# Kernel optimization log

Hardware: AMD Instinct MI355X
Metric: run time of the kernel (lower is better)

Reference implementation:

```python
import jax, jax.numpy as jnp
import numpy as np

S, B, K, H = 2048, 256, 64, 128  # seq_len, batch, process_dim, hidden_size


def softplus10(x):
    return jax.nn.softplus(10.0 * x) / 10.0


def setup_inputs() -> dict:
    key = jax.random.key(0)
    ks = jax.random.split(key, 10)
    sc = 0.1
    dt = jax.random.uniform(ks[0], (S, B), dtype=jnp.float32)
    seq_types = jax.random.randint(ks[1], (S, B), 0, K)  # in [0, K); K is padding idx
    h0 = jnp.zeros((B, H), dtype=jnp.float32)
    embed_W = jax.random.normal(ks[2], (K + 1, K), dtype=jnp.float32) * sc
    embed_W = embed_W.at[K].set(0.0)  # padding_idx row is zero
    W_ih = jax.random.normal(ks[3], (H, K), dtype=jnp.float32) * sc
    b_ih = jax.random.normal(ks[4], (H,), dtype=jnp.float32) * sc
    W_hh = jax.random.normal(ks[5], (H, H), dtype=jnp.float32) * sc
    b_hh = jax.random.normal(ks[6], (H,), dtype=jnp.float32) * sc
    dec_W = jax.random.normal(ks[7], (H, K + H), dtype=jnp.float32) * sc
    dec_b = jax.random.normal(ks[8], (H,), dtype=jnp.float32) * sc
    return {"dt": dt, "h0": h0, "embed_W": embed_W, "W_ih": W_ih, "b_ih": b_ih,
            "W_hh": W_hh, "b_hh": b_hh, "dec_W": dec_W, "dec_b": dec_b,
            "seq_types": seq_types}


def reference(dt, h0, embed_W, W_ih, b_ih, W_hh, b_hh, dec_W, dec_b, seq_types):
    # Per-event recurrence: h(t) = hidden_i * exp(-decay_i * dt_i)
    def step(h, inp):
        dt_t, ty_t = inp                     # [B], [B]
        x = embed_W[ty_t]                    # [B, K] embedding lookup
        concat = jnp.concatenate([x, h], axis=1)          # [B, K+H]
        decay = softplus10(concat @ dec_W.T + dec_b)      # [B, H]
        hidden = jnp.tanh(x @ W_ih.T + b_ih + h @ W_hh.T + b_hh)  # RNNCell tanh
        h_new = hidden * jnp.exp(-decay * dt_t[:, None])  # decayed hidden state
        return h_new, (hidden, decay, h_new)

    _, (hiddens, decays, hiddens_ti) = jax.lax.scan(step, h0, (dt, seq_types))
    # each: [S, B, H], matching the per-step lists of the torch module
    return hiddens, decays, hiddens_ti
```

## Files before the change

kernel.cpp:

```cpp
#include <hip/hip_runtime.h>

#define SEQ 2048
#define BAT 256
#define KD  64
#define HD  128
#define SBH 67108864u

typedef _Float16 half2v  __attribute__((ext_vector_type(2)));
typedef __fp16   fp16x2  __attribute__((ext_vector_type(2)));

template<int PAT>
__device__ __forceinline__ float swz(float x) {
    return __int_as_float(__builtin_amdgcn_ds_swizzle(__float_as_int(x), PAT));
}
#define XOR4 0x101F

template<int CTRL>
__device__ __forceinline__ float dpp_add(float keep, float send) {
    const int r = __builtin_amdgcn_update_dpp(0, __float_as_int(send),
                                              CTRL, 0xF, 0xF, true);
    return keep + __int_as_float(r);
}
template<int CTRL>
__device__ __forceinline__ float dpp_mov(float send) {
    const int r = __builtin_amdgcn_update_dpp(0, __float_as_int(send),
                                              CTRL, 0xF, 0xF, true);
    return __int_as_float(r);
}

__device__ __forceinline__ int PK(float a, float b) {
    fp16x2 p = __builtin_amdgcn_cvt_pkrtz(a, b);
    return __builtin_bit_cast(int, p);
}

__device__ __forceinline__ float fdot2(int w, int h, float c) {
#if __has_builtin(__builtin_amdgcn_fdot2)
    return __builtin_amdgcn_fdot2(__builtin_bit_cast(half2v, w),
                                  __builtin_bit_cast(half2v, h), c, false);
#else
    half2v wv = __builtin_bit_cast(half2v, w), hv = __builtin_bit_cast(half2v, h);
    return fmaf((float)wv[1], (float)hv[1], fmaf((float)wv[0], (float)hv[0], c));
#endif
}

#define PIN(x) asm volatile("" : "+v"(x))
#define PIN4(v4) PIN(v4.x); PIN(v4.y); PIN(v4.z); PIN(v4.w)

#define STEP_BARRIER() do {                                   \
    asm volatile("s_waitcnt lgkmcnt(0)" ::: "memory");        \
    __builtin_amdgcn_s_barrier();                             \
    asm volatile("" ::: "memory");                            \
} while (0)

__global__ __launch_bounds__(128) void precompute_tables(
    const float* __restrict__ embed_W, const float* __restrict__ W_ih,
    const float* __restrict__ b_ih,    const float* __restrict__ b_hh,
    const float* __restrict__ dec_W,   const float* __restrict__ dec_b,
    float* __restrict__ tabH, float* __restrict__ tabD)
{
    __shared__ float x[KD];
    const int ty = blockIdx.x;
    const int r  = threadIdx.x;
    if (r < KD) x[r] = embed_W[ty * KD + r];
    __syncthreads();
    float ah = 0.f, ad = 0.f;
#pragma unroll
    for (int k = 0; k < KD; ++k) {
        const float xv = x[k];
        ah += xv * W_ih[r * KD + k];
        ad += xv * dec_W[r * (KD + HD) + k];
    }
    tabH[ty * HD + r] = ah + b_ih[r] + b_hh[r];
    tabD[ty * HD + r] = ad + dec_b[r];
}

__global__ __launch_bounds__(256, 1) void hawkes_rnn(
    const float* __restrict__ dt_g,  const float* __restrict__ h0,
    const float* __restrict__ W_hh,  const float* __restrict__ dec_W,
    const int*   __restrict__ seq_types,
    const float* __restrict__ tabH,  const float* __restrict__ tabD,
    float* __restrict__ out)
{
    __shared__ __align__(16) _Float16 h16[2][HD];
    __shared__ __align__(8) int2 dtty[SEQ + 2];

    const int b    = blockIdx.x;
    const int tid  = threadIdx.x;
    const int lane = tid & 63;
    const int b0 = lane & 1, b1 = (lane >> 1) & 1;
    const int b2 = (lane >> 2) & 1, b3 = (lane >> 3) & 1;
    const int g    = (tid >> 6) * 4 + (lane >> 4);
    const int row  = 8 * g + 4 * b0 + 2 * b1 + b2;
    const int chunk = b0 | (b1 << 1) | (b2 << 2);

    for (int t = tid; t < SEQ; t += 256) {
        dtty[t] = make_int2(__float_as_int(dt_g[(size_t)t * BAT + b]),
                            seq_types[(size_t)t * BAT + b]);
    }
    if (tid < 2) dtty[SEQ + tid] = make_int2(0, 0);
    if (tid < HD) h16[0][tid] = (_Float16)h0[b * HD + tid];

    const size_t rstr = b3 ? (size_t)(KD + HD) : (size_t)HD;
    const float* wb = (b3 ? (dec_W + KD) : W_hh) + (size_t)(8 * g) * rstr
                      + chunk * 16;
#define LWROW(DA, DB, P) { \
    const float4 _a = *reinterpret_cast<const float4*>(P);        \
    const float4 _b = *reinterpret_cast<const float4*>((P) + 4);  \
    const float4 _c = *reinterpret_cast<const float4*>((P) + 8);  \
    const float4 _d = *reinterpret_cast<const float4*>((P) + 12); \
    DA = make_int4(PK(_a.x,_a.y), PK(_a.z,_a.w), PK(_b.x,_b.y), PK(_b.z,_b.w)); \
    DB = make_int4(PK(_c.x,_c.y), PK(_c.z,_c.w), PK(_d.x,_d.y), PK(_d.z,_d.w)); }
    int4 w0a,w0b,w1a,w1b,w2a,w2b,w3a,w3b,w4a,w4b,w5a,w5b,w6a,w6b,w7a,w7b;
    LWROW(w0a,w0b, wb + 0 * rstr)  LWROW(w1a,w1b, wb + 1 * rstr)
    LWROW(w2a,w2b, wb + 2 * rstr)  LWROW(w3a,w3b, wb + 3 * rstr)
    LWROW(w4a,w4b, wb + 4 * rstr)  LWROW(w5a,w5b, wb + 5 * rstr)
    LWROW(w6a,w6b, wb + 6 * rstr)  LWROW(w7a,w7b, wb + 7 * rstr)
#undef LWROW
    PIN4(w0a); PIN4(w0b); PIN4(w1a); PIN4(w1b);
    PIN4(w2a); PIN4(w2b); PIN4(w3a); PIN4(w3b);
    PIN4(w4a); PIN4(w4b); PIN4(w5a); PIN4(w5b);
    PIN4(w6a); PIN4(w6b); PIN4(w7a); PIN4(w7b);

    const float* tabp = (b3 ? tabD : tabH) + row;

    unsigned off = (unsigned)(b * HD + row);

    __syncthreads();

    int2 pr_cur = dtty[0];
    int2 pr_nxt = dtty[1];
    float tab_cur = tabp[pr_cur.y * HD];
    float tab_nxt = tabp[pr_nxt.y * HD];

#define DOT16(A, WA, WB) \
    A = fdot2(WA.x, hv0.x, A); A = fdot2(WA.y, hv0.y, A); \
    A = fdot2(WA.z, hv0.z, A); A = fdot2(WA.w, hv0.w, A); \
    A = fdot2(WB.x, hv1.x, A); A = fdot2(WB.y, hv1.y, A); \
    A = fdot2(WB.z, hv1.z, A); A = fdot2(WB.w, hv1.w, A);

#define STEP(P, TT) { \
    const int2 pr_pf = dtty[(TT) + 2];                \
    const float tab_pf = tabp[pr_pf.y * HD];          \
    const float dtv = __int_as_float(pr_cur.x); \
     \
    const int4 hv0 = *reinterpret_cast<const int4*>(&h16[P][chunk * 16]); \
    const int4 hv1 = *reinterpret_cast<const int4*>(&h16[P][chunk * 16 + 8]); \
    float a0 = 0.f, a1 = 0.f, a2 = 0.f, a3 = 0.f; \
    float a4 = 0.f, a5 = 0.f, a6 = 0.f, a7 = 0.f; \
    DOT16(a0, w0a, w0b)  DOT16(a1, w1a, w1b) \
    DOT16(a2, w2a, w2b)  DOT16(a3, w3a, w3b) \
    DOT16(a4, w4a, w4b)  DOT16(a5, w5a, w5b) \
    DOT16(a6, w6a, w6b)  DOT16(a7, w7a, w7b) \
     \
    const float t0 = dpp_add<0xB1>(b0 ? a4 : a0, b0 ? a0 : a4); \
    const float t1 = dpp_add<0xB1>(b0 ? a5 : a1, b0 ? a1 : a5); \
    const float t2 = dpp_add<0xB1>(b0 ? a6 : a2, b0 ? a2 : a6); \
    const float t3 = dpp_add<0xB1>(b0 ? a7 : a3, b0 ? a3 : a7); \
     \
    const float u0 = dpp_add<0x4E>(b1 ? t2 : t0, b1 ? t0 : t2); \
    const float u1 = dpp_add<0x4E>(b1 ? t3 : t1, b1 ? t1 : t3); \
     \
    const float snd = b2 ? u0 : u1; \
    const float sv  = (b2 ? u1 : u0) + swz<XOR4>(snd) + tab_cur; \
     \
    const float e2 = __expf(2.f * sv); \
    const float vh = 1.f - __fdividef(2.f, e2 + 1.f);             \
    const float z  = 10.f * sv; \
    const float em = __expf(-fabsf(z)); \
    const float sp = 0.1f * (fmaxf(z, 0.f) + __logf(1.f + em));   \
    const float vd = __expf(-sp * dtv); \
    const float v  = b3 ? vd : vh; \
     \
    const float cross = dpp_mov<0x128>(v); \
    const float hnew  = v * cross; \
    if (b3 == 0) { \
        h16[(P) ^ 1][row] = (_Float16)hnew;    \
        out[off] = v; \
        out[off + 2u * SBH] = hnew; \
    } else { \
        out[off + SBH] = sp; \
    } \
    off += BAT * HD; \
    pr_cur = pr_nxt;   pr_nxt = pr_pf; \
    tab_cur = tab_nxt; tab_nxt = tab_pf; \
    STEP_BARRIER(); \
}

    for (int t = 0; t < SEQ; t += 2) {
        STEP(0, t)
        STEP(1, t + 1)
    }
#undef STEP
#undef DOT16
}

extern "C" void kernel_launch(void* const* d_in, const int* in_sizes, int n_in,
                              void* d_out, int out_size, void* d_ws, size_t ws_size,
                              hipStream_t stream) {
    const float* dt        = (const float*)d_in[0];
    const float* h0        = (const float*)d_in[1];
    const float* embed_W   = (const float*)d_in[2];
    const float* W_ih      = (const float*)d_in[3];
    const float* b_ih      = (const float*)d_in[4];
    const float* W_hh      = (const float*)d_in[5];
    const float* b_hh      = (const float*)d_in[6];
    const float* dec_W     = (const float*)d_in[7];
    const float* dec_b     = (const float*)d_in[8];
    const int*   seq_types = (const int*)  d_in[9];
    float* out  = (float*)d_out;

    float* tabHw = (float*)d_ws;
    float* tabDw = tabHw + (KD + 1) * HD;

    precompute_tables<<<KD + 1, 128, 0, stream>>>(embed_W, W_ih, b_ih, b_hh,
                                                  dec_W, dec_b, tabHw, tabDw);
    hawkes_rnn<<<BAT, 256, 0, stream>>>(dt, h0, W_hh, dec_W, seq_types,
                                        tabHw, tabDw, out);
}
```

Baseline: 972.3 us.

## Remap lane roles, replace swizzle with DPP row-shr, stage tables in LDS as fp16

Reassigns lane bits so the hidden/decay split sits on lane bit 5 and the third reduction stage uses a DPP row shift instead of a ds_swizzle. The hidden/decay exchange now goes through permlane32_swap, falling back to ds_bpermute when that builtin is missing. The precomputed bias tables are copied into shared memory as fp16, so the per-step table fetch hits LDS instead of global memory. The tables lose precision in fp16, and if permlane32_swap is unavailable the bpermute fallback adds an LDS-path exchange on the critical chain.

```diff
diff --git a/kernel.cpp b/kernel.cpp
--- a/kernel.cpp
+++ b/kernel.cpp
@@ -8,12 +8,7 @@
 
 typedef _Float16 half2v  __attribute__((ext_vector_type(2)));
 typedef __fp16   fp16x2  __attribute__((ext_vector_type(2)));
-
-template<int PAT>
-__device__ __forceinline__ float swz(float x) {
-    return __int_as_float(__builtin_amdgcn_ds_swizzle(__float_as_int(x), PAT));
-}
-#define XOR4 0x101F
+typedef unsigned uint2v  __attribute__((ext_vector_type(2)));
 
 template<int CTRL>
 __device__ __forceinline__ float dpp_add(float keep, float send) {
@@ -21,11 +16,17 @@
                                               CTRL, 0xF, 0xF, true);
     return keep + __int_as_float(r);
 }
-template<int CTRL>
-__device__ __forceinline__ float dpp_mov(float send) {
-    const int r = __builtin_amdgcn_update_dpp(0, __float_as_int(send),
-                                              CTRL, 0xF, 0xF, true);
-    return __int_as_float(r);
+
+__device__ __forceinline__ float xchg32(float v, int hi_half, int lane) {
+#if __has_builtin(__builtin_amdgcn_permlane32_swap)
+    uint2v r = __builtin_amdgcn_permlane32_swap(__float_as_uint(v),
+                                                __float_as_uint(v),
+                                                false, false);
+    return __uint_as_float(hi_half ? r.x : r.y);
+#else
+    return __uint_as_float(__builtin_amdgcn_ds_bpermute(
+        ((lane ^ 32) << 2), __float_as_uint(v)));
+#endif
 }
 
 __device__ __forceinline__ int PK(float a, float b) {
@@ -83,25 +84,32 @@
 {
     __shared__ __align__(16) _Float16 h16[2][HD];
     __shared__ __align__(8) int2 dtty[SEQ + 2];
+    __shared__ _Float16 tabLH[(KD + 1) * HD];
+    __shared__ _Float16 tabLD[(KD + 1) * HD];
 
     const int b    = blockIdx.x;
     const int tid  = threadIdx.x;
     const int lane = tid & 63;
     const int b0 = lane & 1, b1 = (lane >> 1) & 1;
     const int b2 = (lane >> 2) & 1, b3 = (lane >> 3) & 1;
-    const int g    = (tid >> 6) * 4 + (lane >> 4);
-    const int row  = 8 * g + 4 * b0 + 2 * b1 + b2;
-    const int chunk = b0 | (b1 << 1) | (b2 << 2);
+    const int b4 = (lane >> 4) & 1, b5 = (lane >> 5) & 1;
+    const int G     = (tid >> 6) * 4 + b4 * 2 + b2;
+    const int row   = 8 * G + 4 * b0 + 2 * b1 + b3;
+    const int chunk = b0 | (b1 << 1) | (b3 << 2);
 
     for (int t = tid; t < SEQ; t += 256) {
         dtty[t] = make_int2(__float_as_int(dt_g[(size_t)t * BAT + b]),
                             seq_types[(size_t)t * BAT + b]);
     }
     if (tid < 2) dtty[SEQ + tid] = make_int2(0, 0);
+    for (int i = tid; i < (KD + 1) * HD; i += 256) {
+        tabLH[i] = (_Float16)tabH[i];
+        tabLD[i] = (_Float16)tabD[i];
+    }
     if (tid < HD) h16[0][tid] = (_Float16)h0[b * HD + tid];
 
-    const size_t rstr = b3 ? (size_t)(KD + HD) : (size_t)HD;
-    const float* wb = (b3 ? (dec_W + KD) : W_hh) + (size_t)(8 * g) * rstr
+    const size_t rstr = b5 ? (size_t)(KD + HD) : (size_t)HD;
+    const float* wb = (b5 ? (dec_W + KD) : W_hh) + (size_t)(8 * G) * rstr
                       + chunk * 16;
 #define LWROW(DA, DB, P) { \
     const float4 _a = *reinterpret_cast<const float4*>(P);        \
@@ -121,7 +129,7 @@
     PIN4(w4a); PIN4(w4b); PIN4(w5a); PIN4(w5b);
     PIN4(w6a); PIN4(w6b); PIN4(w7a); PIN4(w7b);
 
-    const float* tabp = (b3 ? tabD : tabH) + row;
+    const _Float16* tabp = (b5 ? tabLD : tabLH) + row;
 
     unsigned off = (unsigned)(b * HD + row);
 
@@ -129,8 +137,8 @@
 
     int2 pr_cur = dtty[0];
     int2 pr_nxt = dtty[1];
-    float tab_cur = tabp[pr_cur.y * HD];
-    float tab_nxt = tabp[pr_nxt.y * HD];
+    float tab_cur = (float)tabp[pr_cur.y * HD];
+    float tab_nxt = (float)tabp[pr_nxt.y * HD];
 
 #define DOT16(A, WA, WB) \
     A = fdot2(WA.x, hv0.x, A); A = fdot2(WA.y, hv0.y, A); \
@@ -140,7 +148,7 @@
 
 #define STEP(P, TT) { \
     const int2 pr_pf = dtty[(TT) + 2];                \
-    const float tab_pf = tabp[pr_pf.y * HD];          \
+    const float tab_pf = (float)tabp[pr_pf.y * HD];   \
     const float dtv = __int_as_float(pr_cur.x); \
      \
     const int4 hv0 = *reinterpret_cast<const int4*>(&h16[P][chunk * 16]); \
@@ -160,8 +168,7 @@
     const float u0 = dpp_add<0x4E>(b1 ? t2 : t0, b1 ? t0 : t2); \
     const float u1 = dpp_add<0x4E>(b1 ? t3 : t1, b1 ? t1 : t3); \
      \
-    const float snd = b2 ? u0 : u1; \
-    const float sv  = (b2 ? u1 : u0) + swz<XOR4>(snd) + tab_cur; \
+    const float sv = dpp_add<0x128>(b3 ? u1 : u0, b3 ? u0 : u1) + tab_cur; \
      \
     const float e2 = __expf(2.f * sv); \
     const float vh = 1.f - __fdividef(2.f, e2 + 1.f);             \
@@ -169,11 +176,11 @@
     const float em = __expf(-fabsf(z)); \
     const float sp = 0.1f * (fmaxf(z, 0.f) + __logf(1.f + em));   \
     const float vd = __expf(-sp * dtv); \
-    const float v  = b3 ? vd : vh; \
-     \
-    const float cross = dpp_mov<0x128>(v); \
+    const float v  = b5 ? vd : vh; \
+     \
+    const float cross = xchg32(v, b5, lane); \
     const float hnew  = v * cross; \
-    if (b3 == 0) { \
+    if (b5 == 0) { \
         h16[(P) ^ 1][row] = (_Float16)hnew;    \
         out[off] = v; \
         out[off + 2u * SBH] = hnew; \
```

New measurement: 824.4 us. 1.18x faster.
